# Kernel tuning notes

Measured on AMD Instinct MI355X. Metric: run time of the kernel, lower is better.

Reference implementation:

```python
import jax, jax.numpy as jnp
import numpy as np

D_MODEL, N_HEADS, N_KV, THETA = 2048, 16, 4, 10000.0
HEAD_DIM = D_MODEL // N_HEADS  # 128


def _rope_sin_cos(seq_len, head_dim, theta):
    inv_freq = 1.0 / theta ** (jnp.arange(0, head_dim, 2, dtype=jnp.float32) / head_dim)
    pos = jnp.arange(seq_len, dtype=jnp.float32)
    freqs = pos[:, None] * inv_freq[None, :]              # [S, hd/2]
    emb = jnp.concatenate([freqs, freqs], axis=-1)        # [S, hd]
    return jnp.sin(emb), jnp.cos(emb)


def _rotate_half(t):
    h = t.shape[-1] // 2
    return jnp.concatenate([-t[..., h:], t[..., :h]], axis=-1)


def _apply_rope(t, sin, cos):
    # t: [B, H, S, hd]; sin/cos: [S, hd]
    return t * cos[None, None] + _rotate_half(t) * sin[None, None]


def setup_inputs() -> dict:
    key = jax.random.key(0)
    ks = jax.random.split(key, 5)
    B, S = 4, 2048
    scale = 1.0 / np.sqrt(D_MODEL)
    return {
        "x": jax.random.normal(ks[0], (B, S, D_MODEL), jnp.float32),
        "Wq": jax.random.normal(ks[1], (D_MODEL, N_HEADS * HEAD_DIM), jnp.float32) * scale,
        "Wk": jax.random.normal(ks[2], (D_MODEL, N_KV * HEAD_DIM), jnp.float32) * scale,
        "Wv": jax.random.normal(ks[3], (D_MODEL, N_KV * HEAD_DIM), jnp.float32) * scale,
        "Wo": jax.random.normal(ks[4], (N_HEADS * HEAD_DIM, D_MODEL), jnp.float32) * scale,
    }


def reference(x, Wq, Wk, Wv, Wo):
    B, S, _ = x.shape
    G = N_HEADS // N_KV  # query heads per kv head

    q = (x @ Wq).reshape(B, S, N_HEADS, HEAD_DIM).transpose(0, 2, 1, 3)  # [B,H,S,hd]
    k = (x @ Wk).reshape(B, S, N_KV, HEAD_DIM).transpose(0, 2, 1, 3)     # [B,KV,S,hd]
    v = (x @ Wv).reshape(B, S, N_KV, HEAD_DIM).transpose(0, 2, 1, 3)

    sin, cos = _rope_sin_cos(S, HEAD_DIM, THETA)
    q = _apply_rope(q, sin, cos)
    k = _apply_rope(k, sin, cos)

    # grouped attention: avoid materializing repeated kv heads
    qg = q.reshape(B, N_KV, G, S, HEAD_DIM)
    scores = jnp.einsum("bkgqd,bksd->bkgqs", qg, k) / np.sqrt(HEAD_DIM)
    causal = jnp.tril(jnp.ones((S, S), dtype=bool))
    scores = jnp.where(causal[None, None, None], scores, jnp.finfo(scores.dtype).min)
    attn = jax.nn.softmax(scores, axis=-1)
    out = jnp.einsum("bkgqs,bksd->bkgqd", attn, v)          # [B,KV,G,S,hd]
    out = out.reshape(B, N_HEADS, S, HEAD_DIM).transpose(0, 2, 1, 3).reshape(B, S, N_HEADS * HEAD_DIM)
    return out @ Wo
```

## Files before the change

### kernel.cpp

```cpp
#include <hip/hip_runtime.h>
#include <hip/hip_bf16.h>

#define DMODEL 2048
#define NHEADS 16
#define NKV 4
#define HD 128
#define SEQ 2048
#define BATCH 4

typedef __attribute__((ext_vector_type(4))) float f32x4;
typedef __attribute__((ext_vector_type(8))) short bf16x8;

static __device__ __forceinline__ float bf2f(short u) {
    unsigned int x = ((unsigned int)(unsigned short)u) << 16;
    return __builtin_bit_cast(float, x);
}
static __device__ __forceinline__ short f2bf(float f) {
    unsigned int x = __builtin_bit_cast(unsigned int, f);
    unsigned int r = (x + 0x7fffu + ((x >> 16) & 1u)) >> 16;
    return (short)r;
}
static __device__ __forceinline__ unsigned int cvtpk_bf16(float lo, float hi) {
    unsigned int r;
    asm("v_cvt_pk_bf16_f32 %0, %1, %2" : "=v"(r) : "v"(lo), "v"(hi));
    return r;
}
static __device__ __forceinline__ void gload16(const void* g, void* l) {
    __builtin_amdgcn_global_load_lds((const __attribute__((address_space(1))) void*)g,
                                     (__attribute__((address_space(3))) void*)l, 16, 0, 0);
}
static __device__ __forceinline__ void wbar6() {
    asm volatile("s_waitcnt vmcnt(6)" ::: "memory");
    __builtin_amdgcn_s_barrier();
    asm volatile("" ::: "memory");
}
static __device__ __forceinline__ void wbar4() {
    asm volatile("s_waitcnt vmcnt(4)" ::: "memory");
    __builtin_amdgcn_s_barrier();
    asm volatile("" ::: "memory");
}
static __device__ __forceinline__ void bar() {
    __builtin_amdgcn_s_barrier();
    asm volatile("" ::: "memory");
}

__global__ __launch_bounds__(256)
void conv_x(const float* __restrict__ in, short* __restrict__ out, int n8) {
    for (int i = blockIdx.x * blockDim.x + threadIdx.x; i < n8;
         i += gridDim.x * blockDim.x) {
        float4 a = ((const float4*)in)[(size_t)i * 2];
        float4 b = ((const float4*)in)[(size_t)i * 2 + 1];
        bf16x8 o;
        o[0] = f2bf(a.x); o[1] = f2bf(a.y); o[2] = f2bf(a.z); o[3] = f2bf(a.w);
        o[4] = f2bf(b.x); o[5] = f2bf(b.y); o[6] = f2bf(b.z); o[7] = f2bf(b.w);
        ((bf16x8*)out)[i] = o;
    }
}

__global__ __launch_bounds__(256)
void tkern(const float* __restrict__ W, short* __restrict__ Wt, int R, int C) {
    __shared__ short Ts[64 * 72];
    const int tid = threadIdx.x;
    const int r0 = blockIdx.y * 64, c0 = blockIdx.x * 64;
    for (int it = 0; it < 4; ++it) {
        int idx = it * 256 + tid;
        int row = idx >> 4, col4 = (idx & 15) * 4;
        float4 t = *(const float4*)&W[(size_t)(r0 + row) * C + c0 + col4];
        Ts[(col4 + 0) * 72 + row] = f2bf(t.x);
        Ts[(col4 + 1) * 72 + row] = f2bf(t.y);
        Ts[(col4 + 2) * 72 + row] = f2bf(t.z);
        Ts[(col4 + 3) * 72 + row] = f2bf(t.w);
    }
    __syncthreads();
    for (int it = 0; it < 2; ++it) {
        int idx = it * 256 + tid;
        int n = idx >> 3, k8 = (idx & 7) * 8;
        bf16x8 o = *(const bf16x8*)&Ts[n * 72 + k8];
        *(bf16x8*)&Wt[(size_t)(c0 + n) * R + r0 + k8] = o;
    }
}

template <bool C_F32>
__global__ __launch_bounds__(256, 2)
void gemm_sb(const short* __restrict__ A, const short* __restrict__ B,
             void* __restrict__ Cp, int M, int N, int K, int nbx) {
    __shared__ short As[256 * 64];
    __shared__ short Bs[128 * 64];
    const int tid = threadIdx.x, lane = tid & 63, w = tid >> 6;
    const int wr = w >> 1, wc = w & 1, lr = lane & 15, lg = lane >> 4;

    const int nwg = gridDim.x;
    const int qq = nwg >> 3, rr = nwg & 7;
    const int xcd = blockIdx.x & 7, loc = blockIdx.x >> 3;
    const int wg = (xcd < rr ? xcd * (qq + 1) : rr * (qq + 1) + (xcd - rr) * qq) + loc;
    const int m0 = (wg / nbx) * 256, n0 = (wg % nbx) * 128;

    const int srcchunk = ((lane & 7) ^ (lane >> 3)) * 8;
    const int lrow = w * 8;
    const int grow = w * 8 + (lane >> 3);

#define STG_A(T, HA)                                                              \
    {                                                                             \
        _Pragma("unroll") for (int i = 0; i < 4; ++i)                             \
            gload16(&A[(size_t)(m0 + (HA) * 128 + i * 32 + grow) * K +            \
                       (size_t)(T) * 64 + srcchunk],                              \
                    &As[((HA) * 128 + i * 32 + lrow) * 64]);                      \
    }
#define STG_B(T, HB)                                                              \
    {                                                                             \
        _Pragma("unroll") for (int i = 0; i < 2; ++i)                             \
            gload16(&B[(size_t)(n0 + (HB) * 64 + i * 32 + grow) * K +             \
                       (size_t)(T) * 64 + srcchunk],                              \
                    &Bs[((HB) * 64 + i * 32 + lrow) * 64]);                       \
    }

    f32x4 acc[2][4][2][2] = {};
    const int NT = K >> 6;

    STG_A(0, 0);
    STG_B(0, 0);
    STG_B(0, 1);
    STG_A(0, 1);

    bf16x8 af0[4][2], af1[4][2], bf0[2][2], bf1[2][2];
    for (int kt = 0; kt < NT; ++kt) {
        const int Tn = (kt + 1 < NT) ? kt + 1 : kt;

        wbar6();
#pragma unroll
        for (int q = 0; q < 4; ++q)
#pragma unroll
            for (int kk = 0; kk < 2; ++kk)
                af0[q][kk] = *(const bf16x8*)&As[(wr * 64 + q * 16 + lr) * 64 +
                                                 (((kk * 4 + lg) ^ (lr & 7)) << 3)];
#pragma unroll
        for (int r = 0; r < 2; ++r)
#pragma unroll
            for (int kk = 0; kk < 2; ++kk)
                bf0[r][kk] = *(const bf16x8*)&Bs[(wc * 32 + r * 16 + lr) * 64 +
                                                 (((kk * 4 + lg) ^ (lr & 7)) << 3)];
        __builtin_amdgcn_s_setprio(1);
#pragma unroll
        for (int q = 0; q < 4; ++q)
#pragma unroll
            for (int r = 0; r < 2; ++r)
#pragma unroll
                for (int kk = 0; kk < 2; ++kk)
                    acc[0][q][0][r] = __builtin_amdgcn_mfma_f32_16x16x32_bf16(
                        af0[q][kk], bf0[r][kk], acc[0][q][0][r], 0, 0, 0);
        __builtin_amdgcn_s_setprio(0);

        wbar4();
#pragma unroll
        for (int r = 0; r < 2; ++r)
#pragma unroll
            for (int kk = 0; kk < 2; ++kk)
                bf1[r][kk] = *(const bf16x8*)&Bs[(64 + wc * 32 + r * 16 + lr) * 64 +
                                                 (((kk * 4 + lg) ^ (lr & 7)) << 3)];
        STG_A(Tn, 0);
        STG_B(Tn, 0);
        __builtin_amdgcn_s_setprio(1);
#pragma unroll
        for (int q = 0; q < 4; ++q)
#pragma unroll
            for (int r = 0; r < 2; ++r)
#pragma unroll
                for (int kk = 0; kk < 2; ++kk)
                    acc[0][q][1][r] = __builtin_amdgcn_mfma_f32_16x16x32_bf16(
                        af0[q][kk], bf1[r][kk], acc[0][q][1][r], 0, 0, 0);
        __builtin_amdgcn_s_setprio(0);

        wbar6();
#pragma unroll
        for (int q = 0; q < 4; ++q)
#pragma unroll
            for (int kk = 0; kk < 2; ++kk)
                af1[q][kk] = *(const bf16x8*)&As[(128 + wr * 64 + q * 16 + lr) * 64 +
                                                 (((kk * 4 + lg) ^ (lr & 7)) << 3)];
        STG_B(Tn, 1);
        __builtin_amdgcn_s_setprio(1);
#pragma unroll
        for (int q = 0; q < 4; ++q)
#pragma unroll
            for (int r = 0; r < 2; ++r)
#pragma unroll
                for (int kk = 0; kk < 2; ++kk)
                    acc[1][q][0][r] = __builtin_amdgcn_mfma_f32_16x16x32_bf16(
                        af1[q][kk], bf0[r][kk], acc[1][q][0][r], 0, 0, 0);
        __builtin_amdgcn_s_setprio(0);

        bar();
        STG_A(Tn, 1);
        __builtin_amdgcn_s_setprio(1);
#pragma unroll
        for (int q = 0; q < 4; ++q)
#pragma unroll
            for (int r = 0; r < 2; ++r)
#pragma unroll
                for (int kk = 0; kk < 2; ++kk)
                    acc[1][q][1][r] = __builtin_amdgcn_mfma_f32_16x16x32_bf16(
                        af1[q][kk], bf1[r][kk], acc[1][q][1][r], 0, 0, 0);
        __builtin_amdgcn_s_setprio(0);
    }
    asm volatile("s_waitcnt vmcnt(0)" ::: "memory");

#pragma unroll
    for (int hA = 0; hA < 2; ++hA)
#pragma unroll
        for (int q = 0; q < 4; ++q)
#pragma unroll
            for (int hB = 0; hB < 2; ++hB)
#pragma unroll
                for (int r = 0; r < 2; ++r)
#pragma unroll
                    for (int j = 0; j < 4; ++j) {
                        int row = m0 + hA * 128 + wr * 64 + q * 16 + lg * 4 + j;
                        int col = n0 + hB * 64 + wc * 32 + r * 16 + lr;
                        float v = acc[hA][q][hB][r][j];
                        if (C_F32) ((float*)Cp)[(size_t)row * N + col] = v;
                        else ((short*)Cp)[(size_t)row * N + col] = f2bf(v);
                    }
#undef STG_A
#undef STG_B
}

template <bool A_F32, bool C_F32>
__global__ __launch_bounds__(256)
void gemm_kernel(const void* __restrict__ Ap, const float* __restrict__ Bp,
                 void* __restrict__ Cp, int M, int N, int K) {
    const int BK = 32, PAD = 8, LDT = BK + PAD;
    __shared__ short As[128 * LDT];
    __shared__ short Bt[128 * LDT];
    const int tid = threadIdx.x;
    const int lane = tid & 63, w = tid >> 6;
    const int wr = w >> 1, wc = w & 1;
    const int lr = lane & 15, lg = lane >> 4;
    const int m0 = blockIdx.y * 128, n0 = blockIdx.x * 128;
    f32x4 acc[4][4] = {};

    for (int k0 = 0; k0 < K; k0 += BK) {
        __syncthreads();
        for (int it = 0; it < 4; ++it) {
            int row = (tid >> 3) + it * 32;
            int kk = (tid & 7) * 4;
            short4 o;
            if (A_F32) {
                const float* A = (const float*)Ap;
                float4 t = *(const float4*)&A[(size_t)(m0 + row) * K + k0 + kk];
                o.x = f2bf(t.x); o.y = f2bf(t.y); o.z = f2bf(t.z); o.w = f2bf(t.w);
            } else {
                const short* A = (const short*)Ap;
                o = *(const short4*)&A[(size_t)(m0 + row) * K + k0 + kk];
            }
            *(short4*)&As[row * LDT + kk] = o;
        }
        for (int it = 0; it < 4; ++it) {
            int krow = (tid >> 5) + it * 8;
            int col = (tid & 31) * 4;
            float4 t = *(const float4*)&Bp[(size_t)(k0 + krow) * N + n0 + col];
            Bt[(col + 0) * LDT + krow] = f2bf(t.x);
            Bt[(col + 1) * LDT + krow] = f2bf(t.y);
            Bt[(col + 2) * LDT + krow] = f2bf(t.z);
            Bt[(col + 3) * LDT + krow] = f2bf(t.w);
        }
        __syncthreads();
        bf16x8 af[4], bfr[4];
        for (int rb = 0; rb < 4; ++rb)
            af[rb] = *(const bf16x8*)&As[(wr * 64 + rb * 16 + lr) * LDT + lg * 8];
        for (int cb = 0; cb < 4; ++cb)
            bfr[cb] = *(const bf16x8*)&Bt[(wc * 64 + cb * 16 + lr) * LDT + lg * 8];
        for (int rb = 0; rb < 4; ++rb)
            for (int cb = 0; cb < 4; ++cb)
                acc[rb][cb] = __builtin_amdgcn_mfma_f32_16x16x32_bf16(
                    af[rb], bfr[cb], acc[rb][cb], 0, 0, 0);
    }

    for (int rb = 0; rb < 4; ++rb)
        for (int cb = 0; cb < 4; ++cb)
            for (int j = 0; j < 4; ++j) {
                int row = m0 + wr * 64 + rb * 16 + lg * 4 + j;
                int col = n0 + wc * 64 + cb * 16 + lr;
                float v = acc[rb][cb][j];
                if (C_F32) ((float*)Cp)[(size_t)row * N + col] = v;
                else ((short*)Cp)[(size_t)row * N + col] = f2bf(v);
            }
}

__global__ __launch_bounds__(256)
void rope_kernel(short* __restrict__ Qp, int ldq, short* __restrict__ Kp, int ldk) {
    const int QP = BATCH * SEQ * NHEADS * 64;
    const int KP = BATCH * SEQ * NKV * 64;
    const int total = QP + KP;
    const float kscale = 0.08838834764831845f;
    for (int idx = blockIdx.x * blockDim.x + threadIdx.x; idx < total;
         idx += gridDim.x * blockDim.x) {
        short* base;
        size_t off;
        int i, row;
        float scl;
        if (idx < QP) {
            i = idx & 63;
            int hh = (idx >> 6) & (NHEADS - 1);
            row = idx >> 10;
            base = Qp;
            off = (size_t)row * ldq + hh * HD;
            scl = 1.0f;
        } else {
            int t = idx - QP;
            i = t & 63;
            int hh = (t >> 6) & (NKV - 1);
            row = t >> 8;
            base = Kp;
            off = (size_t)row * ldk + hh * HD;
            scl = kscale;
        }
        int pos = row & (SEQ - 1);
        float invf = exp2f(-(float)i * (13.287712379549449f / 64.0f));
        float ang = (float)pos * invf;
        float s, c;
        sincosf(ang, &s, &c);
        float t1 = bf2f(base[off + i]);
        float t2 = bf2f(base[off + i + 64]);
        base[off + i] = f2bf((t1 * c - t2 * s) * scl);
        base[off + i + 64] = f2bf((t2 * c + t1 * s) * scl);
    }
}

__global__ __launch_bounds__(512, 2)
void attn_kernel(const short* __restrict__ Qp, int ldq,
                 const short* __restrict__ Kp, int ldk,
                 const short* __restrict__ Vp, int ldv,
                 short* __restrict__ O) {
    __shared__ short Ks[2][64 * 128];
    __shared__ short Vt[128 * 64];
    __shared__ short Pw[8][16 * 64];

    const int tid = threadIdx.x, lane = tid & 63, w = tid >> 6;
    const int lr = lane & 15, lg = lane >> 4;
    const int h = blockIdx.y, b = blockIdx.z;
    const int kvh = h >> 2;
    const size_t brow = (size_t)b * SEQ;

    const int d0 = (tid & 15) * 8;
    const int rvb = (tid >> 4) * 2;
    bf16x8 vreg[2];

#define STAGE_K(T, BUF)                                                              \
    {                                                                                \
        _Pragma("unroll") for (int it = 0; it < 2; ++it) {                           \
            int row = w * 8 + it * 4 + (lane >> 4);                                  \
            int cblk = (lane & 15) ^ (row & 7);                                      \
            gload16(&Kp[(brow + (size_t)(T) * 64 + row) * ldk + kvh * HD + cblk * 8],\
                    &Ks[BUF][(w * 8 + it * 4) * 128]);                               \
        }                                                                            \
    }
#define LOAD_V(T)                                                                    \
    {                                                                                \
        _Pragma("unroll") for (int h2 = 0; h2 < 2; ++h2)                             \
            vreg[h2] = *(const bf16x8*)&Vp[(brow + (size_t)(T) * 64 + rvb + h2) *    \
                                           ldv + kvh * HD + d0];                     \
    }
#define WRITE_V()                                                                    \
    {                                                                                \
        _Pragma("unroll") for (int e = 0; e < 8; ++e) {                              \
            int d = d0 + e;                                                          \
            int g = (e ^ lr) & 7;                                                    \
            unsigned int pk = ((unsigned int)(unsigned short)vreg[0][e]) |           \
                              (((unsigned int)(unsigned short)vreg[1][e]) << 16);    \
            *(unsigned int*)&Vt[d * 64 + (((rvb >> 3) ^ g) << 3) + (rvb & 7)] = pk;  \
        }                                                                            \
    }

    for (int pass = 0; pass < 2; ++pass) {
        const int qt = (pass == 0) ? (int)blockIdx.x : 7 - (int)blockIdx.x;
        const int q0 = qt * 256;
        const int qrow_g[2] = {q0 + w * 32 + lr, q0 + w * 32 + 16 + lr};

        bf16x8 qf[2][4];
#pragma unroll
        for (int g = 0; g < 2; ++g)
#pragma unroll
            for (int kc = 0; kc < 4; ++kc)
                qf[g][kc] = *(const bf16x8*)&Qp[(brow + qrow_g[g]) * ldq + h * HD +
                                                kc * 32 + lg * 8];

        f32x4 oacc[2][8] = {};
        float mrun[2] = {-__builtin_inff(), -__builtin_inff()};
        float lrun[2] = {0.f, 0.f};

        const int ntiles = 4 * qt + 4;

        STAGE_K(0, 0);
        LOAD_V(0);
        __syncthreads();
        WRITE_V();
        __syncthreads();

        int cur = 0;
        for (int t = 0; t < ntiles; ++t) {
            const int kv0 = t * 64;
            const int nxt = cur ^ 1;
            const bool pre = (t + 1 < ntiles);
            if (pre) {
                if (nxt) { STAGE_K(t + 1, 1); } else { STAGE_K(t + 1, 0); }
                LOAD_V(t + 1);
            }

#pragma unroll
            for (int g = 0; g < 2; ++g) {
                const int qrow = qrow_g[g];
                f32x4 sacc[4] = {};
                __builtin_amdgcn_s_setprio(1);
#pragma unroll
                for (int cb = 0; cb < 4; ++cb)
#pragma unroll
                    for (int kc = 0; kc < 4; ++kc) {
                        bf16x8 kf = *(const bf16x8*)&Ks[cur][(cb * 16 + lr) * 128 +
                                                             (((kc * 4 + lg) ^ (lr & 7)) << 3)];
                        sacc[cb] = __builtin_amdgcn_mfma_f32_16x16x32_bf16(
                            kf, qf[g][kc], sacc[cb], 0, 0, 0);
                    }
                __builtin_amdgcn_s_setprio(0);

                float st[16];
                const bool need_mask = (kv0 + 63 > qrow);
#pragma unroll
                for (int cb = 0; cb < 4; ++cb)
#pragma unroll
                    for (int j = 0; j < 4; ++j) {
                        float s = sacc[cb][j];
                        if (need_mask) {
                            int col = kv0 + cb * 16 + lg * 4 + j;
                            if (col > qrow) s = -__builtin_inff();
                        }
                        st[cb * 4 + j] = s;
                    }
                float m8[8], m4[4];
#pragma unroll
                for (int i = 0; i < 8; ++i) m8[i] = fmaxf(st[i], st[i + 8]);
#pragma unroll
                for (int i = 0; i < 4; ++i) m4[i] = fmaxf(m8[i], m8[i + 4]);
                float rowmax = fmaxf(fmaxf(m4[0], m4[1]), fmaxf(m4[2], m4[3]));
                rowmax = fmaxf(rowmax, __shfl_xor(rowmax, 16, 64));
                rowmax = fmaxf(rowmax, __shfl_xor(rowmax, 32, 64));

                if (!__all(rowmax <= mrun[g] + 8.f)) {
                    float mnew = fmaxf(mrun[g], rowmax);
                    float alpha = __expf(mrun[g] - mnew);
                    lrun[g] *= alpha;
#pragma unroll
                    for (int db = 0; db < 8; ++db) {
                        f32x4 o = oacc[g][db];
#pragma unroll
                        for (int j = 0; j < 4; ++j) o[j] *= alpha;
                        oacc[g][db] = o;
                    }
                    mrun[g] = mnew;
                }
                const float mbase = mrun[g];
#pragma unroll
                for (int i = 0; i < 16; ++i) st[i] = __expf(st[i] - mbase);
                float s8[8], s4[4];
#pragma unroll
                for (int i = 0; i < 8; ++i) s8[i] = st[i] + st[i + 8];
#pragma unroll
                for (int i = 0; i < 4; ++i) s4[i] = s8[i] + s8[i + 4];
                float rs = (s4[0] + s4[1]) + (s4[2] + s4[3]);
                rs += __shfl_xor(rs, 16, 64);
                rs += __shfl_xor(rs, 32, 64);
                lrun[g] += rs;

#pragma unroll
                for (int cb = 0; cb < 4; ++cb) {
                    uint2 pk2;
                    pk2.x = cvtpk_bf16(st[cb * 4 + 0], st[cb * 4 + 1]);
                    pk2.y = cvtpk_bf16(st[cb * 4 + 2], st[cb * 4 + 3]);
                    int chunk = (cb * 2 + (lg >> 1)) ^ (lr & 7);
                    *(uint2*)&Pw[w][lr * 64 + (chunk << 3) + (lg & 1) * 4] = pk2;
                }
                bf16x8 pf[2];
#pragma unroll
                for (int kc = 0; kc < 2; ++kc)
                    pf[kc] = *(const bf16x8*)&Pw[w][lr * 64 +
                                                   (((kc * 4 + lg) ^ (lr & 7)) << 3)];

                __builtin_amdgcn_s_setprio(1);
#pragma unroll
                for (int db = 0; db < 8; ++db)
#pragma unroll
                    for (int kc = 0; kc < 2; ++kc) {
                        int d = db * 16 + lr;
                        int gg = ((lr & 7) ^ (db * 2 + (lr >> 3))) & 7;
                        bf16x8 vf = *(const bf16x8*)&Vt[d * 64 + (((kc * 4 + lg) ^ gg) << 3)];
                        oacc[g][db] = __builtin_amdgcn_mfma_f32_16x16x32_bf16(
                            vf, pf[kc], oacc[g][db], 0, 0, 0);
                    }
                __builtin_amdgcn_s_setprio(0);
            }

            if (pre) {
                __syncthreads();
                WRITE_V();
                __syncthreads();
                cur = nxt;
            }
        }

#pragma unroll
        for (int g = 0; g < 2; ++g) {
            const float invl = 1.0f / lrun[g];
#pragma unroll
            for (int db = 0; db < 8; ++db) {
                short4 o4;
                o4.x = f2bf(oacc[g][db][0] * invl);
                o4.y = f2bf(oacc[g][db][1] * invl);
                o4.z = f2bf(oacc[g][db][2] * invl);
                o4.w = f2bf(oacc[g][db][3] * invl);
                *(short4*)&O[(brow + qrow_g[g]) * DMODEL + h * HD + db * 16 + lg * 4] = o4;
            }
        }
    }
#undef STAGE_K
#undef LOAD_V
#undef WRITE_V
}

extern "C" void kernel_launch(void* const* d_in, const int* in_sizes, int n_in,
                              void* d_out, int out_size, void* d_ws, size_t ws_size,
                              hipStream_t stream) {
    const float* x = (const float*)d_in[0];
    const float* Wq = (const float*)d_in[1];
    const float* Wk = (const float*)d_in[2];
    const float* Wv = (const float*)d_in[3];
    const float* Wo = (const float*)d_in[4];
    float* out = (float*)d_out;

    const size_t BS = (size_t)BATCH * SEQ;
    dim3 blk(256);

    const size_t planA_shorts = BS * 2048 + BS * 3072 + (size_t)3072 * 2048 + (size_t)2048 * 2048;
    if (ws_size >= planA_shorts * 2) {
        short* xb = (short*)d_ws;
        short* QKV = xb + BS * 2048;
        short* WqkvT = QKV + BS * 3072;
        short* WoT = WqkvT + (size_t)3072 * 2048;
        short* AO = xb;

        conv_x<<<dim3(2048), blk, 0, stream>>>(x, xb, (int)(BS * 2048 / 8));
        tkern<<<dim3(32, 32), blk, 0, stream>>>(Wq, WqkvT, 2048, 2048);
        tkern<<<dim3(8, 32), blk, 0, stream>>>(Wk, WqkvT + (size_t)2048 * 2048, 2048, 512);
        tkern<<<dim3(8, 32), blk, 0, stream>>>(Wv, WqkvT + (size_t)2560 * 2048, 2048, 512);
        tkern<<<dim3(32, 32), blk, 0, stream>>>(Wo, WoT, 2048, 2048);
        gemm_sb<false><<<dim3(768), blk, 0, stream>>>(xb, WqkvT, (void*)QKV,
                                                      8192, 3072, 2048, 24);
        rope_kernel<<<dim3(4096), blk, 0, stream>>>(QKV, 3072, QKV + 2048, 3072);
        attn_kernel<<<dim3(4, NHEADS, BATCH), dim3(512), 0, stream>>>(
            QKV, 3072, QKV + 2048, 3072, QKV + 2560, 3072, AO);
        gemm_sb<true><<<dim3(512), blk, 0, stream>>>(AO, WoT, (void*)out,
                                                     8192, 2048, 2048, 16);
    } else {
        short* Qb = (short*)d_ws;
        short* Kb = Qb + BS * DMODEL;
        short* Vb = Kb + BS * (NKV * HD);
        short* AO = Vb + BS * (NKV * HD);
        gemm_kernel<true, false><<<dim3(16, 64), blk, 0, stream>>>((const void*)x, Wq, (void*)Qb, 8192, 2048, 2048);
        gemm_kernel<true, false><<<dim3(4, 64), blk, 0, stream>>>((const void*)x, Wk, (void*)Kb, 8192, 512, 2048);
        gemm_kernel<true, false><<<dim3(4, 64), blk, 0, stream>>>((const void*)x, Wv, (void*)Vb, 8192, 512, 2048);
        rope_kernel<<<dim3(4096), blk, 0, stream>>>(Qb, 2048, Kb, 512);
        attn_kernel<<<dim3(4, NHEADS, BATCH), dim3(512), 0, stream>>>(
            Qb, 2048, Kb, 512, Vb, 512, AO);
        gemm_kernel<false, true><<<dim3(16, 64), blk, 0, stream>>>((const void*)AO, Wo, (void*)out, 8192, 2048, 2048);
    }
}
```

Measured before the change: 370.4 us.

## Halve attention query tile to one 16-row group per wave, quadruple grid

The attention kernel now processes 128 query rows per block (one 16-row MFMA group per wave) instead of 256, with the grid widened from 4 to 16 blocks along the query axis and causal pairing adjusted to 15-qt. Launch bounds are raised to target 4 blocks per CU. This reduces per-thread registers and raises parallelism and load balance. In exchange, each staged K/V tile feeds half as much compute, increasing K/V global and LDS traffic and barrier overhead per FLOP.

```diff
diff --git a/kernel.cpp b/kernel.cpp
--- a/kernel.cpp
+++ b/kernel.cpp
@@ -326,7 +326,7 @@
     }
 }
 
-__global__ __launch_bounds__(512, 2)
+__global__ __launch_bounds__(512, 4)
 void attn_kernel(const short* __restrict__ Qp, int ldq,
                  const short* __restrict__ Kp, int ldk,
                  const short* __restrict__ Vp, int ldv,
@@ -372,23 +372,19 @@
     }
 
     for (int pass = 0; pass < 2; ++pass) {
-        const int qt = (pass == 0) ? (int)blockIdx.x : 7 - (int)blockIdx.x;
-        const int q0 = qt * 256;
-        const int qrow_g[2] = {q0 + w * 32 + lr, q0 + w * 32 + 16 + lr};
-
-        bf16x8 qf[2][4];
-#pragma unroll
-        for (int g = 0; g < 2; ++g)
-#pragma unroll
-            for (int kc = 0; kc < 4; ++kc)
-                qf[g][kc] = *(const bf16x8*)&Qp[(brow + qrow_g[g]) * ldq + h * HD +
-                                                kc * 32 + lg * 8];
-
-        f32x4 oacc[2][8] = {};
-        float mrun[2] = {-__builtin_inff(), -__builtin_inff()};
-        float lrun[2] = {0.f, 0.f};
-
-        const int ntiles = 4 * qt + 4;
+        const int qt = (pass == 0) ? (int)blockIdx.x : 15 - (int)blockIdx.x;
+        const int q0 = qt * 128;
+        const int qrow = q0 + w * 16 + lr;
+
+        bf16x8 qf[4];
+#pragma unroll
+        for (int kc = 0; kc < 4; ++kc)
+            qf[kc] = *(const bf16x8*)&Qp[(brow + qrow) * ldq + h * HD + kc * 32 + lg * 8];
+
+        f32x4 oacc[8] = {};
+        float mrun = -__builtin_inff(), lrun = 0.f;
+
+        const int ntiles = 2 * qt + 2;
 
         STAGE_K(0, 0);
         LOAD_V(0);
@@ -406,97 +402,92 @@
                 LOAD_V(t + 1);
             }
 
-#pragma unroll
-            for (int g = 0; g < 2; ++g) {
-                const int qrow = qrow_g[g];
-                f32x4 sacc[4] = {};
-                __builtin_amdgcn_s_setprio(1);
-#pragma unroll
-                for (int cb = 0; cb < 4; ++cb)
-#pragma unroll
-                    for (int kc = 0; kc < 4; ++kc) {
-                        bf16x8 kf = *(const bf16x8*)&Ks[cur][(cb * 16 + lr) * 128 +
-                                                             (((kc * 4 + lg) ^ (lr & 7)) << 3)];
-                        sacc[cb] = __builtin_amdgcn_mfma_f32_16x16x32_bf16(
-                            kf, qf[g][kc], sacc[cb], 0, 0, 0);
+            f32x4 sacc[4] = {};
+            __builtin_amdgcn_s_setprio(1);
+#pragma unroll
+            for (int cb = 0; cb < 4; ++cb)
+#pragma unroll
+                for (int kc = 0; kc < 4; ++kc) {
+                    bf16x8 kf = *(const bf16x8*)&Ks[cur][(cb * 16 + lr) * 128 +
+                                                         (((kc * 4 + lg) ^ (lr & 7)) << 3)];
+                    sacc[cb] = __builtin_amdgcn_mfma_f32_16x16x32_bf16(
+                        kf, qf[kc], sacc[cb], 0, 0, 0);
+                }
+            __builtin_amdgcn_s_setprio(0);
+
+            float st[16];
+            const bool need_mask = (kv0 + 63 > qrow);
+#pragma unroll
+            for (int cb = 0; cb < 4; ++cb)
+#pragma unroll
+                for (int j = 0; j < 4; ++j) {
+                    float s = sacc[cb][j];
+                    if (need_mask) {
+                        int col = kv0 + cb * 16 + lg * 4 + j;
+                        if (col > qrow) s = -__builtin_inff();
                     }
-                __builtin_amdgcn_s_setprio(0);
-
-                float st[16];
-                const bool need_mask = (kv0 + 63 > qrow);
-#pragma unroll
-                for (int cb = 0; cb < 4; ++cb)
-#pragma unroll
-                    for (int j = 0; j < 4; ++j) {
-                        float s = sacc[cb][j];
-                        if (need_mask) {
-                            int col = kv0 + cb * 16 + lg * 4 + j;
-                            if (col > qrow) s = -__builtin_inff();
-                        }
-                        st[cb * 4 + j] = s;
-                    }
-                float m8[8], m4[4];
-#pragma unroll
-                for (int i = 0; i < 8; ++i) m8[i] = fmaxf(st[i], st[i + 8]);
-#pragma unroll
-                for (int i = 0; i < 4; ++i) m4[i] = fmaxf(m8[i], m8[i + 4]);
-                float rowmax = fmaxf(fmaxf(m4[0], m4[1]), fmaxf(m4[2], m4[3]));
-                rowmax = fmaxf(rowmax, __shfl_xor(rowmax, 16, 64));
-                rowmax = fmaxf(rowmax, __shfl_xor(rowmax, 32, 64));
-
-                if (!__all(rowmax <= mrun[g] + 8.f)) {
-                    float mnew = fmaxf(mrun[g], rowmax);
-                    float alpha = __expf(mrun[g] - mnew);
-                    lrun[g] *= alpha;
-#pragma unroll
-                    for (int db = 0; db < 8; ++db) {
-                        f32x4 o = oacc[g][db];
-#pragma unroll
-                        for (int j = 0; j < 4; ++j) o[j] *= alpha;
-                        oacc[g][db] = o;
-                    }
-                    mrun[g] = mnew;
+                    st[cb * 4 + j] = s;
                 }
-                const float mbase = mrun[g];
-#pragma unroll
-                for (int i = 0; i < 16; ++i) st[i] = __expf(st[i] - mbase);
-                float s8[8], s4[4];
-#pragma unroll
-                for (int i = 0; i < 8; ++i) s8[i] = st[i] + st[i + 8];
-#pragma unroll
-                for (int i = 0; i < 4; ++i) s4[i] = s8[i] + s8[i + 4];
-                float rs = (s4[0] + s4[1]) + (s4[2] + s4[3]);
-                rs += __shfl_xor(rs, 16, 64);
-                rs += __shfl_xor(rs, 32, 64);
-                lrun[g] += rs;
-
-#pragma unroll
-                for (int cb = 0; cb < 4; ++cb) {
-                    uint2 pk2;
-                    pk2.x = cvtpk_bf16(st[cb * 4 + 0], st[cb * 4 + 1]);
-                    pk2.y = cvtpk_bf16(st[cb * 4 + 2], st[cb * 4 + 3]);
-                    int chunk = (cb * 2 + (lg >> 1)) ^ (lr & 7);
-                    *(uint2*)&Pw[w][lr * 64 + (chunk << 3) + (lg & 1) * 4] = pk2;
+            float m8[8], m4[4];
+#pragma unroll
+            for (int i = 0; i < 8; ++i) m8[i] = fmaxf(st[i], st[i + 8]);
+#pragma unroll
+            for (int i = 0; i < 4; ++i) m4[i] = fmaxf(m8[i], m8[i + 4]);
+            float rowmax = fmaxf(fmaxf(m4[0], m4[1]), fmaxf(m4[2], m4[3]));
+            rowmax = fmaxf(rowmax, __shfl_xor(rowmax, 16, 64));
+            rowmax = fmaxf(rowmax, __shfl_xor(rowmax, 32, 64));
+
+            if (!__all(rowmax <= mrun + 8.f)) {
+                float mnew = fmaxf(mrun, rowmax);
+                float alpha = __expf(mrun - mnew);
+                lrun *= alpha;
+#pragma unroll
+                for (int db = 0; db < 8; ++db) {
+                    f32x4 o = oacc[db];
+#pragma unroll
+                    for (int j = 0; j < 4; ++j) o[j] *= alpha;
+                    oacc[db] = o;
                 }
-                bf16x8 pf[2];
-#pragma unroll
-                for (int kc = 0; kc < 2; ++kc)
-                    pf[kc] = *(const bf16x8*)&Pw[w][lr * 64 +
-                                                   (((kc * 4 + lg) ^ (lr & 7)) << 3)];
-
-                __builtin_amdgcn_s_setprio(1);
-#pragma unroll
-                for (int db = 0; db < 8; ++db)
-#pragma unroll
-                    for (int kc = 0; kc < 2; ++kc) {
-                        int d = db * 16 + lr;
-                        int gg = ((lr & 7) ^ (db * 2 + (lr >> 3))) & 7;
-                        bf16x8 vf = *(const bf16x8*)&Vt[d * 64 + (((kc * 4 + lg) ^ gg) << 3)];
-                        oacc[g][db] = __builtin_amdgcn_mfma_f32_16x16x32_bf16(
-                            vf, pf[kc], oacc[g][db], 0, 0, 0);
-                    }
-                __builtin_amdgcn_s_setprio(0);
+                mrun = mnew;
             }
+#pragma unroll
+            for (int i = 0; i < 16; ++i) st[i] = __expf(st[i] - mrun);
+            float s8[8], s4[4];
+#pragma unroll
+            for (int i = 0; i < 8; ++i) s8[i] = st[i] + st[i + 8];
+#pragma unroll
+            for (int i = 0; i < 4; ++i) s4[i] = s8[i] + s8[i + 4];
+            float rs = (s4[0] + s4[1]) + (s4[2] + s4[3]);
+            rs += __shfl_xor(rs, 16, 64);
+            rs += __shfl_xor(rs, 32, 64);
+            lrun += rs;
+
+#pragma unroll
+            for (int cb = 0; cb < 4; ++cb) {
+                uint2 pk2;
+                pk2.x = cvtpk_bf16(st[cb * 4 + 0], st[cb * 4 + 1]);
+                pk2.y = cvtpk_bf16(st[cb * 4 + 2], st[cb * 4 + 3]);
+                int chunk = (cb * 2 + (lg >> 1)) ^ (lr & 7);
+                *(uint2*)&Pw[w][lr * 64 + (chunk << 3) + (lg & 1) * 4] = pk2;
+            }
+            bf16x8 pf[2];
+#pragma unroll
+            for (int kc = 0; kc < 2; ++kc)
+                pf[kc] = *(const bf16x8*)&Pw[w][lr * 64 +
+                                               (((kc * 4 + lg) ^ (lr & 7)) << 3)];
+
+            __builtin_amdgcn_s_setprio(1);
+#pragma unroll
+            for (int db = 0; db < 8; ++db)
+#pragma unroll
+                for (int kc = 0; kc < 2; ++kc) {
+                    int d = db * 16 + lr;
+                    int gg = ((lr & 7) ^ (db * 2 + (lr >> 3))) & 7;
+                    bf16x8 vf = *(const bf16x8*)&Vt[d * 64 + (((kc * 4 + lg) ^ gg) << 3)];
+                    oacc[db] = __builtin_amdgcn_mfma_f32_16x16x32_bf16(
+                        vf, pf[kc], oacc[db], 0, 0, 0);
+                }
+            __builtin_amdgcn_s_setprio(0);
 
             if (pre) {
                 __syncthreads();
@@ -506,18 +497,15 @@
             }
         }
 
-#pragma unroll
-        for (int g = 0; g < 2; ++g) {
-            const float invl = 1.0f / lrun[g];
-#pragma unroll
-            for (int db = 0; db < 8; ++db) {
-                short4 o4;
-                o4.x = f2bf(oacc[g][db][0] * invl);
-                o4.y = f2bf(oacc[g][db][1] * invl);
-                o4.z = f2bf(oacc[g][db][2] * invl);
-                o4.w = f2bf(oacc[g][db][3] * invl);
-                *(short4*)&O[(brow + qrow_g[g]) * DMODEL + h * HD + db * 16 + lg * 4] = o4;
-            }
+        const float invl = 1.0f / lrun;
+#pragma unroll
+        for (int db = 0; db < 8; ++db) {
+            short4 o4;
+            o4.x = f2bf(oacc[db][0] * invl);
+            o4.y = f2bf(oacc[db][1] * invl);
+            o4.z = f2bf(oacc[db][2] * invl);
+            o4.w = f2bf(oacc[db][3] * invl);
+            *(short4*)&O[(brow + qrow) * DMODEL + h * HD + db * 16 + lg * 4] = o4;
         }
     }
 #undef STAGE_K
@@ -554,7 +542,7 @@
         gemm_sb<false><<<dim3(768), blk, 0, stream>>>(xb, WqkvT, (void*)QKV,
                                                       8192, 3072, 2048, 24);
         rope_kernel<<<dim3(4096), blk, 0, stream>>>(QKV, 3072, QKV + 2048, 3072);
-        attn_kernel<<<dim3(4, NHEADS, BATCH), dim3(512), 0, stream>>>(
+        attn_kernel<<<dim3(16, NHEADS, BATCH), dim3(512), 0, stream>>>(
             QKV, 3072, QKV + 2048, 3072, QKV + 2560, 3072, AO);
         gemm_sb<true><<<dim3(512), blk, 0, stream>>>(AO, WoT, (void*)out,
                                                      8192, 2048, 2048, 16);
@@ -567,7 +555,7 @@
         gemm_kernel<true, false><<<dim3(4, 64), blk, 0, stream>>>((const void*)x, Wk, (void*)Kb, 8192, 512, 2048);
         gemm_kernel<true, false><<<dim3(4, 64), blk, 0, stream>>>((const void*)x, Wv, (void*)Vb, 8192, 512, 2048);
         rope_kernel<<<dim3(4096), blk, 0, stream>>>(Qb, 2048, Kb, 512);
-        attn_kernel<<<dim3(4, NHEADS, BATCH), dim3(512), 0, stream>>>(
+        attn_kernel<<<dim3(16, NHEADS, BATCH), dim3(512), 0, stream>>>(
             Qb, 2048, Kb, 512, Vb, 512, AO);
         gemm_kernel<false, true><<<dim3(16, 64), blk, 0, stream>>>((const void*)AO, Wo, (void*)out, 8192, 2048, 2048);
     }
```

After: 475.6 us. 28.4% more time.
